# Optimization experiments

Hardware: AMD Instinct MI355X
Metric: run time of the kernel (lower is better)

Reference implementation:

```python
import jax, jax.numpy as jnp
import numpy as np

B, S, E, H = 2, 2048, 1024, 16
D = E // H  # head_dim = 64


def setup_inputs() -> dict:
    key = jax.random.key(0)
    ks = jax.random.split(key, 6)
    sc = 0.02
    return {
        "hidden_states": jax.random.normal(ks[0], (B, S, E), dtype=jnp.float32),
        "attn_bias": jax.random.normal(ks[1], (S, S), dtype=jnp.float32) * sc,
        "Wqkv": jax.random.normal(ks[2], (E, 3 * E), dtype=jnp.float32) * sc,
        "bqkv": jax.random.normal(ks[3], (3 * E,), dtype=jnp.float32) * sc,
        "Wproj": jax.random.normal(ks[4], (E, E), dtype=jnp.float32) * sc,
        "bproj": jax.random.normal(ks[5], (E,), dtype=jnp.float32) * sc,
    }


def reference(hidden_states, attn_bias, Wqkv, bqkv, Wproj, bproj):
    b, s, e = hidden_states.shape
    qkv = hidden_states @ Wqkv + bqkv                      # [b,s,3e]
    q, k, v = jnp.split(qkv, 3, axis=-1)                   # each [b,s,e]
    cache_key, cache_value = k, v                          # kvCache
    # [b,h,s,d]
    qh = q.reshape(b, s, H, D).transpose(0, 2, 1, 3)
    kh = k.reshape(b, s, H, D).transpose(0, 2, 1, 3)
    vh = v.reshape(b, s, H, D).transpose(0, 2, 1, 3)
    scores = jnp.einsum("bhqd,bhkd->bhqk", qh, kh) / jnp.sqrt(jnp.float32(D))
    scores = scores + attn_bias[:s, :s][None, None]        # learned additive bias
    causal = jnp.tril(jnp.ones((s, s), dtype=bool))
    scores = jnp.where(causal[None, None], scores, jnp.float32(-1e9))
    attn = jax.nn.softmax(scores, axis=-1)
    ctx = jnp.einsum("bhqk,bhkd->bhqd", attn, vh)
    ctx = ctx.transpose(0, 2, 1, 3).reshape(b, s, e)
    out = ctx @ Wproj + bproj                              # resid dropout p=0 -> identity
    return (out, cache_key, cache_value)
```

## Files before the change

kernel.cpp:

```cpp
#include <hip/hip_runtime.h>

#define B_ 2
#define S_ 2048
#define E_ 1024
#define H_ 16
#define D_ 64

typedef short  s16x8 __attribute__((ext_vector_type(8)));
typedef float  f32x4 __attribute__((ext_vector_type(4)));
typedef unsigned short u16x4 __attribute__((ext_vector_type(4)));

__device__ __forceinline__ ushort f2bf(float f) {
    union { float f; unsigned u; } x; x.f = f;
    unsigned u = x.u + 0x7fffu + ((x.u >> 16) & 1u);
    return (ushort)(u >> 16);
}

__global__ __launch_bounds__(256) void cvtx_kernel(
    const float* __restrict__ X, ushort* __restrict__ Xbf)
{
    int i = (blockIdx.x * 256 + threadIdx.x) * 4;
    float4 v = *(const float4*)&X[i];
    u16x4 o;
    o.x = f2bf(v.x); o.y = f2bf(v.y); o.z = f2bf(v.z); o.w = f2bf(v.w);
    *(u16x4*)&Xbf[i] = o;
}

__global__ __launch_bounds__(256) void wtrans_kernel(
    const float* __restrict__ W, ushort* __restrict__ Wt, int Kdim, int Ndim)
{
    __shared__ float tile[64][65];
    int n0 = blockIdx.x * 64, k0 = blockIdx.y * 64;
    int tid = threadIdx.x;
    int c = tid & 63;
#pragma unroll
    for (int r = tid >> 6; r < 64; r += 4)
        tile[r][c] = W[(size_t)(k0 + r) * Ndim + n0 + c];
    __syncthreads();
#pragma unroll
    for (int r = tid >> 6; r < 64; r += 4)
        Wt[(size_t)(n0 + r) * Kdim + k0 + c] = f2bf(tile[c][r]);
}

__global__ __launch_bounds__(256) void gemm_mfma_bt(
    const ushort* __restrict__ A,
    const ushort* __restrict__ Bt,
    const float* __restrict__ bias,
    int M, int N, int K,
    float* __restrict__ C0,
    ushort* __restrict__ Qbf, float* __restrict__ Kf32, ushort* __restrict__ Kbf,
    float* __restrict__ Vf32, int mode)
{
    __shared__ ushort As[128 * 32];
    __shared__ ushort Bs[128 * 32];
    int tid = threadIdx.x;
    int wid = tid >> 6, lane = tid & 63;
    int l15 = lane & 15, quad = lane >> 4;
    int wm = wid >> 1, wn = wid & 1;
    int row0 = blockIdx.y * 128, col0 = blockIdx.x * 128;

    int sr = wid * 16 + (lane >> 2);
    int sk = (lane & 3) * 8;

    f32x4 acc[4][4];
#pragma unroll
    for (int mt = 0; mt < 4; mt++)
#pragma unroll
        for (int nt = 0; nt < 4; nt++) acc[mt][nt] = (f32x4){0.f, 0.f, 0.f, 0.f};

    for (int k0 = 0; k0 < K; k0 += 32) {
        __syncthreads();
#pragma unroll
        for (int c = 0; c < 2; c++) {
            int r = c * 64 + sr;
            __builtin_amdgcn_global_load_lds(
                (const __attribute__((address_space(1))) unsigned int*)
                    &A[(size_t)(row0 + r) * K + k0 + sk],
                (__attribute__((address_space(3))) unsigned int*)&As[r * 32 + sk],
                16, 0, 0);
            __builtin_amdgcn_global_load_lds(
                (const __attribute__((address_space(1))) unsigned int*)
                    &Bt[(size_t)(col0 + r) * K + k0 + sk],
                (__attribute__((address_space(3))) unsigned int*)&Bs[r * 32 + sk],
                16, 0, 0);
        }
        __syncthreads();

        s16x8 af[4], bf[4];
#pragma unroll
        for (int mt = 0; mt < 4; mt++)
            af[mt] = *(const s16x8*)&As[(wm * 64 + mt * 16 + l15) * 32 + quad * 8];
#pragma unroll
        for (int nt = 0; nt < 4; nt++)
            bf[nt] = *(const s16x8*)&Bs[(wn * 64 + nt * 16 + l15) * 32 + quad * 8];
#pragma unroll
        for (int mt = 0; mt < 4; mt++)
#pragma unroll
            for (int nt = 0; nt < 4; nt++)
                acc[mt][nt] = __builtin_amdgcn_mfma_f32_16x16x32_bf16(
                    af[mt], bf[nt], acc[mt][nt], 0, 0, 0);
    }

#pragma unroll
    for (int nt = 0; nt < 4; nt++) {
        int n = col0 + wn * 64 + nt * 16 + l15;
        float bv = bias[n];
        if (mode == 1) {
            int seg = n >> 10;
            int nn = n & (E_ - 1);
#pragma unroll
            for (int mt = 0; mt < 4; mt++)
#pragma unroll
                for (int r = 0; r < 4; r++) {
                    int row = row0 + wm * 64 + mt * 16 + quad * 4 + r;
                    float v = acc[mt][nt][r] + bv;
                    size_t idx = (size_t)row * E_ + nn;
                    if (seg == 0)      Qbf[idx] = f2bf(v);
                    else if (seg == 1) { Kf32[idx] = v; Kbf[idx] = f2bf(v); }
                    else               Vf32[idx] = v;
                }
        } else {
#pragma unroll
            for (int mt = 0; mt < 4; mt++)
#pragma unroll
                for (int r = 0; r < 4; r++) {
                    int row = row0 + wm * 64 + mt * 16 + quad * 4 + r;
                    C0[(size_t)row * N + n] = acc[mt][nt][r] + bv;
                }
        }
    }
}

__global__ __launch_bounds__(256) void vtrans_kernel(
    const float* __restrict__ V, ushort* __restrict__ Vt)
{
    __shared__ float tile[64][65];
    int blk = blockIdx.x;
    int s0 = (blk & 31) * 64;
    int bh = blk >> 5;
    int b = bh >> 4, h = bh & 15;
    int tid = threadIdx.x;
    int d = tid & 63;
#pragma unroll
    for (int i = tid >> 6; i < 64; i += 4)
        tile[i][d] = V[((size_t)(b * S_ + s0 + i)) * E_ + h * 64 + d];
    __syncthreads();
    int lane = tid & 63, w = tid >> 6;
#pragma unroll
    for (int dd = w; dd < 64; dd += 4)
        Vt[((size_t)(bh * 64 + dd)) * S_ + s0 + lane] = f2bf(tile[lane][dd]);
}

__global__ __launch_bounds__(256) void attn_mfma_kernel(
    const ushort* __restrict__ Qbf,
    const ushort* __restrict__ Kbf,
    const ushort* __restrict__ Vt,
    const float* __restrict__ bias,
    ushort* __restrict__ Ctx)
{
    __shared__ ushort Ks[64][72];
    __shared__ ushort Vs[64][72];
    __shared__ ushort Ps[4][16][72];

    int blk = blockIdx.x;
    int bh = blk & 31;
    int qt = 31 - (blk >> 5);
    int b = bh >> 4, h = bh & 15;
    int tid = threadIdx.x;
    int wid = tid >> 6, lane = tid & 63;
    int l15 = lane & 15, quad = lane >> 4;

    int q0w = qt * 64 + wid * 16;

    const size_t qbase = ((size_t)(b * S_ + q0w + l15)) * E_ + h * 64 + quad * 8;
    s16x8 qa0 = *(const s16x8*)&Qbf[qbase];
    s16x8 qa1 = *(const s16x8*)&Qbf[qbase + 32];

    f32x4 o[4];
#pragma unroll
    for (int dt = 0; dt < 4; dt++) o[dt] = (f32x4){0.f, 0.f, 0.f, 0.f};
    float lsum[4];
#pragma unroll
    for (int r = 0; r < 4; r++) lsum[r] = 0.f;

    int skey = tid >> 2;
    int scol = (tid & 3) * 16;
    const float scale = 0.125f;

    for (int t = 0; t <= qt; t++) {
        int j0 = t * 64;
        __syncthreads();
        {
            const float4* ksrc = (const float4*)&Kbf[((size_t)(b * S_ + j0 + skey)) * E_ + h * 64 + scol];
            float4 k0 = ksrc[0], k1 = ksrc[1];
            *(float4*)&Ks[skey][scol]     = k0;
            *(float4*)&Ks[skey][scol + 8] = k1;
            const float4* vsrc = (const float4*)&Vt[((size_t)(bh * 64 + skey)) * S_ + j0 + scol];
            float4 v0 = vsrc[0], v1 = vsrc[1];
            *(float4*)&Vs[skey][scol]     = v0;
            *(float4*)&Vs[skey][scol + 8] = v1;
        }
        __syncthreads();

        float bv[4][4];
#pragma unroll
        for (int r = 0; r < 4; r++)
#pragma unroll
            for (int kt = 0; kt < 4; kt++)
                bv[r][kt] = bias[(size_t)(q0w + quad * 4 + r) * S_ + j0 + kt * 16 + l15];

        f32x4 s[4];
#pragma unroll
        for (int kt = 0; kt < 4; kt++) {
            s16x8 kb0 = *(const s16x8*)&Ks[kt * 16 + l15][quad * 8];
            s16x8 kb1 = *(const s16x8*)&Ks[kt * 16 + l15][quad * 8 + 32];
            f32x4 acc = (f32x4){0.f, 0.f, 0.f, 0.f};
            acc = __builtin_amdgcn_mfma_f32_16x16x32_bf16(qa0, kb0, acc, 0, 0, 0);
            acc = __builtin_amdgcn_mfma_f32_16x16x32_bf16(qa1, kb1, acc, 0, 0, 0);
            s[kt] = acc;
        }

        bool diag = (t == qt);
#pragma unroll
        for (int r = 0; r < 4; r++) {
            int row = q0w + quad * 4 + r;
#pragma unroll
            for (int kt = 0; kt < 4; kt++) {
                int j = j0 + kt * 16 + l15;
                float v = s[kt][r] * scale + bv[r][kt];
                float p = (diag && j > row) ? 0.f : __expf(v);
                lsum[r] += p;
                Ps[wid][quad * 4 + r][kt * 16 + l15] = f2bf(p);
            }
        }

        s16x8 pa0 = *(const s16x8*)&Ps[wid][l15][quad * 8];
        s16x8 pa1 = *(const s16x8*)&Ps[wid][l15][quad * 8 + 32];
#pragma unroll
        for (int dt = 0; dt < 4; dt++) {
            s16x8 vb0 = *(const s16x8*)&Vs[dt * 16 + l15][quad * 8];
            s16x8 vb1 = *(const s16x8*)&Vs[dt * 16 + l15][quad * 8 + 32];
            o[dt] = __builtin_amdgcn_mfma_f32_16x16x32_bf16(pa0, vb0, o[dt], 0, 0, 0);
            o[dt] = __builtin_amdgcn_mfma_f32_16x16x32_bf16(pa1, vb1, o[dt], 0, 0, 0);
        }
    }

    float inv_l[4];
#pragma unroll
    for (int r = 0; r < 4; r++) {
        float l = lsum[r];
        l += __shfl_xor(l, 1);
        l += __shfl_xor(l, 2);
        l += __shfl_xor(l, 4);
        l += __shfl_xor(l, 8);
        inv_l[r] = 1.f / l;
    }

#pragma unroll
    for (int dt = 0; dt < 4; dt++) {
#pragma unroll
        for (int r = 0; r < 4; r++) {
            int row = q0w + quad * 4 + r;
            Ctx[((size_t)(b * S_ + row)) * E_ + h * 64 + dt * 16 + l15] =
                f2bf(o[dt][r] * inv_l[r]);
        }
    }
}

extern "C" void kernel_launch(void* const* d_in, const int* in_sizes, int n_in,
                              void* d_out, int out_size, void* d_ws, size_t ws_size,
                              hipStream_t stream) {
    const float* X     = (const float*)d_in[0];
    const float* abias = (const float*)d_in[1];
    const float* Wqkv  = (const float*)d_in[2];
    const float* bqkv  = (const float*)d_in[3];
    const float* Wproj = (const float*)d_in[4];
    const float* bproj = (const float*)d_in[5];

    const size_t plane = (size_t)B_ * S_ * E_;
    float* out  = (float*)d_out;
    float* kout = out + plane;
    float* vout = kout + plane;

    ushort* xbf    = (ushort*)d_ws;
    ushort* qbf    = xbf + plane;
    ushort* kbf    = qbf + plane;
    ushort* vt     = kbf + plane;
    ushort* ctxbf  = xbf;
    ushort* wqkvt  = vt + plane;
    ushort* wprojt = wqkvt + (size_t)3 * E_ * E_;

    const int M = B_ * S_;

    cvtx_kernel<<<dim3(plane / 1024), 256, 0, stream>>>(X, xbf);
    wtrans_kernel<<<dim3(3 * E_ / 64, E_ / 64), 256, 0, stream>>>(Wqkv, wqkvt, E_, 3 * E_);
    wtrans_kernel<<<dim3(E_ / 64, E_ / 64), 256, 0, stream>>>(Wproj, wprojt, E_, E_);

    gemm_mfma_bt<<<dim3(3 * E_ / 128, M / 128), 256, 0, stream>>>(
        xbf, wqkvt, bqkv, M, 3 * E_, E_,
        nullptr, qbf, kout, kbf, vout, 1);

    vtrans_kernel<<<dim3(B_ * H_ * (S_ / 64)), 256, 0, stream>>>(vout, vt);

    attn_mfma_kernel<<<dim3(B_ * H_ * (S_ / 64)), 256, 0, stream>>>(
        qbf, kbf, vt, abias, ctxbf);

    gemm_mfma_bt<<<dim3(E_ / 128, M / 128), 256, 0, stream>>>(
        ctxbf, wprojt, bproj, M, E_, E_,
        out, nullptr, nullptr, nullptr, nullptr, 0);
}
```

Measured before the change: 251.1 us.

## Pair causal query tiles per block, prefetch K/V/bias, swizzle P buffer

Each attention block now handles two query tiles (qt and 31-qt), so every block does the same amount of causal work and the grid shrinks to 512 blocks. The K, V and bias loads for the next key tile are issued into registers while the current tile is being computed, which hides global-memory latency behind the MFMA work. The P staging buffer in shared memory gets an XOR swizzle to cut bank conflicts. With only 512 blocks there is less parallelism across CUs, and the prefetch registers raise register pressure.

```diff
diff --git a/kernel.cpp b/kernel.cpp
--- a/kernel.cpp
+++ b/kernel.cpp
@@ -164,105 +164,129 @@
 
     int blk = blockIdx.x;
     int bh = blk & 31;
-    int qt = 31 - (blk >> 5);
+    int pr = blk >> 5;
     int b = bh >> 4, h = bh & 15;
     int tid = threadIdx.x;
     int wid = tid >> 6, lane = tid & 63;
     int l15 = lane & 15, quad = lane >> 4;
 
-    int q0w = qt * 64 + wid * 16;
-
-    const size_t qbase = ((size_t)(b * S_ + q0w + l15)) * E_ + h * 64 + quad * 8;
-    s16x8 qa0 = *(const s16x8*)&Qbf[qbase];
-    s16x8 qa1 = *(const s16x8*)&Qbf[qbase + 32];
-
-    f32x4 o[4];
-#pragma unroll
-    for (int dt = 0; dt < 4; dt++) o[dt] = (f32x4){0.f, 0.f, 0.f, 0.f};
-    float lsum[4];
-#pragma unroll
-    for (int r = 0; r < 4; r++) lsum[r] = 0.f;
-
     int skey = tid >> 2;
     int scol = (tid & 3) * 16;
     const float scale = 0.125f;
 
-    for (int t = 0; t <= qt; t++) {
-        int j0 = t * 64;
-        __syncthreads();
-        {
-            const float4* ksrc = (const float4*)&Kbf[((size_t)(b * S_ + j0 + skey)) * E_ + h * 64 + scol];
-            float4 k0 = ksrc[0], k1 = ksrc[1];
-            *(float4*)&Ks[skey][scol]     = k0;
-            *(float4*)&Ks[skey][scol + 8] = k1;
-            const float4* vsrc = (const float4*)&Vt[((size_t)(bh * 64 + skey)) * S_ + j0 + scol];
-            float4 v0 = vsrc[0], v1 = vsrc[1];
-            *(float4*)&Vs[skey][scol]     = v0;
-            *(float4*)&Vs[skey][scol + 8] = v1;
-        }
-        __syncthreads();
-
-        float bv[4][4];
+    const size_t krow = (size_t)(b * S_ + skey) * E_ + h * 64 + scol;
+    const size_t vrow = (size_t)(bh * 64 + skey) * S_ + scol;
+
+    for (int half = 0; half < 2; half++) {
+        int qt = half ? pr : (31 - pr);
+        int q0w = qt * 64 + wid * 16;
+
+        const size_t qbase = ((size_t)(b * S_ + q0w + l15)) * E_ + h * 64 + quad * 8;
+        s16x8 qa0 = *(const s16x8*)&Qbf[qbase];
+        s16x8 qa1 = *(const s16x8*)&Qbf[qbase + 32];
+
+        f32x4 o[4];
+#pragma unroll
+        for (int dt = 0; dt < 4; dt++) o[dt] = (f32x4){0.f, 0.f, 0.f, 0.f};
+        float lsum[4];
+#pragma unroll
+        for (int r = 0; r < 4; r++) lsum[r] = 0.f;
+
+        float4 kr0 = ((const float4*)&Kbf[krow])[0];
+        float4 kr1 = ((const float4*)&Kbf[krow])[1];
+        float4 vr0 = ((const float4*)&Vt[vrow])[0];
+        float4 vr1 = ((const float4*)&Vt[vrow])[1];
+        float bvn[4][4];
 #pragma unroll
         for (int r = 0; r < 4; r++)
 #pragma unroll
             for (int kt = 0; kt < 4; kt++)
-                bv[r][kt] = bias[(size_t)(q0w + quad * 4 + r) * S_ + j0 + kt * 16 + l15];
-
-        f32x4 s[4];
-#pragma unroll
-        for (int kt = 0; kt < 4; kt++) {
-            s16x8 kb0 = *(const s16x8*)&Ks[kt * 16 + l15][quad * 8];
-            s16x8 kb1 = *(const s16x8*)&Ks[kt * 16 + l15][quad * 8 + 32];
-            f32x4 acc = (f32x4){0.f, 0.f, 0.f, 0.f};
-            acc = __builtin_amdgcn_mfma_f32_16x16x32_bf16(qa0, kb0, acc, 0, 0, 0);
-            acc = __builtin_amdgcn_mfma_f32_16x16x32_bf16(qa1, kb1, acc, 0, 0, 0);
-            s[kt] = acc;
-        }
-
-        bool diag = (t == qt);
+                bvn[r][kt] = bias[(size_t)(q0w + quad * 4 + r) * S_ + kt * 16 + l15];
+
+        for (int t = 0; t <= qt; t++) {
+            int j0 = t * 64;
+            __syncthreads();
+            *(float4*)&Ks[skey][scol]     = kr0;
+            *(float4*)&Ks[skey][scol + 8] = kr1;
+            *(float4*)&Vs[skey][scol]     = vr0;
+            *(float4*)&Vs[skey][scol + 8] = vr1;
+            float bv[4][4];
+#pragma unroll
+            for (int r = 0; r < 4; r++)
+#pragma unroll
+                for (int kt = 0; kt < 4; kt++) bv[r][kt] = bvn[r][kt];
+            __syncthreads();
+
+            if (t < qt) {
+                int j1 = j0 + 64;
+                kr0 = ((const float4*)&Kbf[krow + (size_t)j1 * E_])[0];
+                kr1 = ((const float4*)&Kbf[krow + (size_t)j1 * E_])[1];
+                vr0 = ((const float4*)&Vt[vrow + j1])[0];
+                vr1 = ((const float4*)&Vt[vrow + j1])[1];
+#pragma unroll
+                for (int r = 0; r < 4; r++)
+#pragma unroll
+                    for (int kt = 0; kt < 4; kt++)
+                        bvn[r][kt] = bias[(size_t)(q0w + quad * 4 + r) * S_ + j1 + kt * 16 + l15];
+            }
+
+            f32x4 s[4];
+#pragma unroll
+            for (int kt = 0; kt < 4; kt++) {
+                s16x8 kb0 = *(const s16x8*)&Ks[kt * 16 + l15][quad * 8];
+                s16x8 kb1 = *(const s16x8*)&Ks[kt * 16 + l15][quad * 8 + 32];
+                f32x4 acc = (f32x4){0.f, 0.f, 0.f, 0.f};
+                acc = __builtin_amdgcn_mfma_f32_16x16x32_bf16(qa0, kb0, acc, 0, 0, 0);
+                acc = __builtin_amdgcn_mfma_f32_16x16x32_bf16(qa1, kb1, acc, 0, 0, 0);
+                s[kt] = acc;
+            }
+
+            bool diag = (t == qt);
+#pragma unroll
+            for (int r = 0; r < 4; r++) {
+                int row = q0w + quad * 4 + r;
+#pragma unroll
+                for (int kt = 0; kt < 4; kt++) {
+                    int j = j0 + kt * 16 + l15;
+                    float v = s[kt][r] * scale + bv[r][kt];
+                    float p = (diag && j > row) ? 0.f : __expf(v);
+                    lsum[r] += p;
+                    int chunk = (kt * 2 + (l15 >> 3)) ^ quad;
+                    Ps[wid][quad * 4 + r][chunk * 8 + (l15 & 7)] = f2bf(p);
+                }
+            }
+
+            int cb = (quad ^ (l15 >> 2)) * 8;
+            s16x8 pa0 = *(const s16x8*)&Ps[wid][l15][cb];
+            s16x8 pa1 = *(const s16x8*)&Ps[wid][l15][cb + 32];
+#pragma unroll
+            for (int dt = 0; dt < 4; dt++) {
+                s16x8 vb0 = *(const s16x8*)&Vs[dt * 16 + l15][quad * 8];
+                s16x8 vb1 = *(const s16x8*)&Vs[dt * 16 + l15][quad * 8 + 32];
+                o[dt] = __builtin_amdgcn_mfma_f32_16x16x32_bf16(pa0, vb0, o[dt], 0, 0, 0);
+                o[dt] = __builtin_amdgcn_mfma_f32_16x16x32_bf16(pa1, vb1, o[dt], 0, 0, 0);
+            }
+        }
+
+        float inv_l[4];
 #pragma unroll
         for (int r = 0; r < 4; r++) {
-            int row = q0w + quad * 4 + r;
-#pragma unroll
-            for (int kt = 0; kt < 4; kt++) {
-                int j = j0 + kt * 16 + l15;
-                float v = s[kt][r] * scale + bv[r][kt];
-                float p = (diag && j > row) ? 0.f : __expf(v);
-                lsum[r] += p;
-                Ps[wid][quad * 4 + r][kt * 16 + l15] = f2bf(p);
-            }
-        }
-
-        s16x8 pa0 = *(const s16x8*)&Ps[wid][l15][quad * 8];
-        s16x8 pa1 = *(const s16x8*)&Ps[wid][l15][quad * 8 + 32];
+            float l = lsum[r];
+            l += __shfl_xor(l, 1);
+            l += __shfl_xor(l, 2);
+            l += __shfl_xor(l, 4);
+            l += __shfl_xor(l, 8);
+            inv_l[r] = 1.f / l;
+        }
+
 #pragma unroll
         for (int dt = 0; dt < 4; dt++) {
-            s16x8 vb0 = *(const s16x8*)&Vs[dt * 16 + l15][quad * 8];
-            s16x8 vb1 = *(const s16x8*)&Vs[dt * 16 + l15][quad * 8 + 32];
-            o[dt] = __builtin_amdgcn_mfma_f32_16x16x32_bf16(pa0, vb0, o[dt], 0, 0, 0);
-            o[dt] = __builtin_amdgcn_mfma_f32_16x16x32_bf16(pa1, vb1, o[dt], 0, 0, 0);
-        }
-    }
-
-    float inv_l[4];
-#pragma unroll
-    for (int r = 0; r < 4; r++) {
-        float l = lsum[r];
-        l += __shfl_xor(l, 1);
-        l += __shfl_xor(l, 2);
-        l += __shfl_xor(l, 4);
-        l += __shfl_xor(l, 8);
-        inv_l[r] = 1.f / l;
-    }
-
-#pragma unroll
-    for (int dt = 0; dt < 4; dt++) {
-#pragma unroll
-        for (int r = 0; r < 4; r++) {
-            int row = q0w + quad * 4 + r;
-            Ctx[((size_t)(b * S_ + row)) * E_ + h * 64 + dt * 16 + l15] =
-                f2bf(o[dt][r] * inv_l[r]);
+#pragma unroll
+            for (int r = 0; r < 4; r++) {
+                int row = q0w + quad * 4 + r;
+                Ctx[((size_t)(b * S_ + row)) * E_ + h * 64 + dt * 16 + l15] =
+                    f2bf(o[dt][r] * inv_l[r]);
+            }
         }
     }
 }
@@ -302,7 +326,7 @@
 
     vtrans_kernel<<<dim3(B_ * H_ * (S_ / 64)), 256, 0, stream>>>(vout, vt);
 
-    attn_mfma_kernel<<<dim3(B_ * H_ * (S_ / 64)), 256, 0, stream>>>(
+    attn_mfma_kernel<<<dim3(B_ * H_ * 16), 256, 0, stream>>>(
         qbf, kbf, vt, abias, ctxbf);
 
     gemm_mfma_bt<<<dim3(E_ / 128, M / 128), 256, 0, stream>>>(
```

New measurement: 238.2 us. 5.1% less time.
